# Optimization experiments

Hardware: AMD Instinct MI355X
Metric: run time of the kernel (lower is better)

## Reference

```python
import jax, jax.numpy as jnp
import numpy as np

D_MODEL = 1024
NUM_HEADS = 16
HEAD_DIM = D_MODEL // NUM_HEADS


def setup_inputs() -> dict:
    key = jax.random.key(0)
    k0, k1, k2, k3, k4 = jax.random.split(key, 5)
    B, S, D = 4, 2048, D_MODEL
    std = np.sqrt(2.0 / (D + D)).astype(np.float32)
    return {
        "in_features": jax.random.normal(k0, (B, S, D), dtype=jnp.float32),
        "Wq": jax.random.normal(k1, (D, D), dtype=jnp.float32) * std,
        "Wk": jax.random.normal(k2, (D, D), dtype=jnp.float32) * std,
        "Wv": jax.random.normal(k3, (D, D), dtype=jnp.float32) * std,
        "Wo": jax.random.normal(k4, (D, D), dtype=jnp.float32) * std,
    }


def reference(in_features, Wq, Wk, Wv, Wo):
    B, S, D = in_features.shape
    H, Hd = NUM_HEADS, HEAD_DIM

    def split_heads(x):  # (B,S,D) -> (B,H,S,Hd)
        return x.reshape(B, S, H, Hd).transpose(0, 2, 1, 3)

    q = split_heads(in_features @ Wq.T)
    k = split_heads(in_features @ Wk.T)
    v = split_heads(in_features @ Wv.T)

    scale = 1.0 / jnp.sqrt(jnp.asarray(Hd, dtype=q.dtype))
    scores = jnp.einsum("bhsd,bhtd->bhst", q, k) * scale  # (B,H,S,S)
    causal = jnp.tril(jnp.ones((S, S), dtype=bool))  # (S,S)
    scores = jnp.where(causal[None, None], scores, -jnp.inf)
    attn = jax.nn.softmax(scores, axis=-1)
    out = jnp.einsum("bhst,bhtd->bhsd", attn, v)  # (B,H,S,Hd)
    out = out.transpose(0, 2, 1, 3).reshape(B, S, D)
    return out @ Wo.T
```

## Files before the change

kernel.cpp:

```cpp
#include <hip/hip_runtime.h>


typedef float f32x4 __attribute__((ext_vector_type(4)));
typedef short s16x8 __attribute__((ext_vector_type(8)));

#if __has_builtin(__builtin_amdgcn_exp2f)
#define EXP2(x) __builtin_amdgcn_exp2f(x)
#else
#define EXP2(x) exp2f(x)
#endif

__device__ __forceinline__ unsigned short f2bf(float f) {
  unsigned int u = __float_as_uint(f);
  u += 0x7fffu + ((u >> 16) & 1u);
  return (unsigned short)(u >> 16);
}

__device__ __forceinline__ unsigned int pk2bf(float f0, float f1) {
  return __builtin_amdgcn_perm(__float_as_uint(f1) + 0x8000u,
                               __float_as_uint(f0) + 0x8000u, 0x07060302u);
}

__device__ __forceinline__ void gl_lds16(const short* g, short* lds) {
  __builtin_amdgcn_global_load_lds(
      (const __attribute__((address_space(1))) unsigned int*)g,
      (__attribute__((address_space(3))) unsigned int*)lds, 16, 0, 0);
}

__global__ __launch_bounds__(256) void cvt_kernel(const float4* __restrict__ s,
                                                  ushort4* __restrict__ d, int n4) {
  int i = blockIdx.x * blockDim.x + threadIdx.x;
  int stride = gridDim.x * blockDim.x;
  for (int idx = i; idx < n4; idx += stride) {
    float4 f = s[idx];
    ushort4 r;
    r.x = f2bf(f.x); r.y = f2bf(f.y); r.z = f2bf(f.z); r.w = f2bf(f.w);
    d[idx] = r;
  }
}

__global__ __launch_bounds__(256) void cvtw_kernel(const float4* __restrict__ w0,
                                                   const float4* __restrict__ w1,
                                                   const float4* __restrict__ w2,
                                                   const float4* __restrict__ w3,
                                                   ushort4* __restrict__ d0,
                                                   ushort4* __restrict__ d1,
                                                   ushort4* __restrict__ d2,
                                                   ushort4* __restrict__ d3) {
  const int n4 = 1024 * 1024 / 4;
  const float4* s;
  ushort4* d;
  switch (blockIdx.y) {
    case 0: s = w0; d = d0; break;
    case 1: s = w1; d = d1; break;
    case 2: s = w2; d = d2; break;
    default: s = w3; d = d3; break;
  }
  int i = blockIdx.x * blockDim.x + threadIdx.x;
  int stride = gridDim.x * blockDim.x;
  for (int idx = i; idx < n4; idx += stride) {
    float4 f = s[idx];
    ushort4 r;
    r.x = f2bf(f.x); r.y = f2bf(f.y); r.z = f2bf(f.z); r.w = f2bf(f.w);
    d[idx] = r;
  }
}

template <int MODE>
__global__ __launch_bounds__(256) void gemm_bt(const short* __restrict__ A,
                                               const short* __restrict__ B,
                                               float* __restrict__ Cf,
                                               short* __restrict__ q_o,
                                               short* __restrict__ k_o,
                                               short* __restrict__ vT_o,
                                               int M, int N, int K) {
  const int tid = threadIdx.x;
  const int wave = tid >> 6, lane = tid & 63;
  const int quad = lane >> 4, l15 = lane & 15;
  const int m0 = blockIdx.x * 128, n0 = blockIdx.y * 128;
  const int wm = (wave >> 1) * 64, wn = (wave & 1) * 64;

  __shared__ __align__(16) short As[128 * 64];
  __shared__ __align__(16) short Bs[128 * 64];

  const f32x4 z4 = {0.f, 0.f, 0.f, 0.f};
  f32x4 acc[4][4];
  for (int i = 0; i < 4; ++i)
    for (int j = 0; j < 4; ++j) acc[i][j] = z4;

  for (int k0 = 0; k0 < K; k0 += 64) {
    __syncthreads();
    for (int i = 0; i < 4; ++i) {
      int c = wave * 4 + i;
      int r = c * 8 + (lane >> 3);
      int c8 = (lane & 7) ^ (r & 7);
      gl_lds16(A + (size_t)(m0 + r) * K + k0 + c8 * 8, As + c * 512 + lane * 8);
      gl_lds16(B + (size_t)(n0 + r) * K + k0 + c8 * 8, Bs + c * 512 + lane * 8);
    }
    __syncthreads();
    for (int kk = 0; kk < 64; kk += 32) {
      int c8b = (kk >> 3) + quad;
      s16x8 af[4], bfr[4];
      for (int mt = 0; mt < 4; ++mt) {
        int row = wm + mt * 16 + l15;
        af[mt] = *(const s16x8*)(As + row * 64 + ((c8b ^ (row & 7)) << 3));
      }
      for (int nt = 0; nt < 4; ++nt) {
        int row = wn + nt * 16 + l15;
        bfr[nt] = *(const s16x8*)(Bs + row * 64 + ((c8b ^ (row & 7)) << 3));
      }
      for (int mt = 0; mt < 4; ++mt)
        for (int nt = 0; nt < 4; ++nt)
          acc[mt][nt] = __builtin_amdgcn_mfma_f32_16x16x32_bf16(af[mt], bfr[nt],
                                                                acc[mt][nt], 0, 0, 0);
    }
  }

  if (MODE == 0) {
    for (int mt = 0; mt < 4; ++mt)
      for (int nt = 0; nt < 4; ++nt) {
        int col = n0 + wn + nt * 16 + l15;
        for (int r = 0; r < 4; ++r) {
          int row = m0 + wm + mt * 16 + quad * 4 + r;
          Cf[(size_t)row * N + col] = acc[mt][nt][r];
        }
      }
  } else {
    if (n0 < 1024) {
      const float scale = 0.18033688011112042f;
      for (int mt = 0; mt < 4; ++mt)
        for (int nt = 0; nt < 4; ++nt) {
          int col = n0 + wn + nt * 16 + l15;
          for (int r = 0; r < 4; ++r) {
            int row = m0 + wm + mt * 16 + quad * 4 + r;
            ((unsigned short*)q_o)[(size_t)row * 1024 + col] = f2bf(acc[mt][nt][r] * scale);
          }
        }
    } else if (n0 < 2048) {
      for (int mt = 0; mt < 4; ++mt)
        for (int nt = 0; nt < 4; ++nt) {
          int col = n0 - 1024 + wn + nt * 16 + l15;
          for (int r = 0; r < 4; ++r) {
            int row = m0 + wm + mt * 16 + quad * 4 + r;
            ((unsigned short*)k_o)[(size_t)row * 1024 + col] = f2bf(acc[mt][nt][r]);
          }
        }
    } else {
      for (int mt = 0; mt < 4; ++mt)
        for (int nt = 0; nt < 4; ++nt) {
          int col = n0 - 2048 + wn + nt * 16 + l15;
          int h = col >> 6, d = col & 63;
          int row0 = m0 + wm + mt * 16 + quad * 4;
          int b = row0 >> 11, s = row0 & 2047;
          uint2 pk;
          pk.x = pk2bf(acc[mt][nt][0], acc[mt][nt][1]);
          pk.y = pk2bf(acc[mt][nt][2], acc[mt][nt][3]);
          *(uint2*)((unsigned short*)vT_o + (((size_t)b * 16 + h) * 64 + d) * 2048 + s) = pk;
        }
    }
  }
}

__global__ __launch_bounds__(256) void attn_kernel(const short* __restrict__ qb,
                                                   const short* __restrict__ kb,
                                                   const short* __restrict__ vT,
                                                   short* __restrict__ ob) {
  const int p = blockIdx.x;
  const int bh = blockIdx.y;
  const int tid = threadIdx.x;
  const int wave = tid >> 6, lane = tid & 63;
  const int quad = lane >> 4, l15 = lane & 15;
  const size_t rowbase = (size_t)(bh >> 4) * 2048;
  const int hoff = (bh & 15) * 64;

  __shared__ __align__(16) short Ks[8192];
  __shared__ __align__(16) short VTs[8192];
  __shared__ __align__(16) short Ps[10240];
  short* Pw = Ps + wave * 2560;

  const f32x4 z4 = {0.f, 0.f, 0.f, 0.f};

  for (int pass = 0; pass < 2; ++pass) {
    const int qt = pass ? p : 15 - p;
    const int q0 = qt * 128;

    s16x8 qf[2][2];
#pragma unroll
    for (int n = 0; n < 2; ++n) {
      const short* qrow = qb + (rowbase + q0 + wave * 32 + n * 16 + l15) * 1024 + hoff;
#pragma unroll
      for (int k2 = 0; k2 < 2; ++k2)
        qf[n][k2] = *(const s16x8*)(qrow + k2 * 32 + quad * 8);
    }

    f32x4 oacc[2][4];
#pragma unroll
    for (int n = 0; n < 2; ++n)
#pragma unroll
      for (int dt = 0; dt < 4; ++dt) oacc[n][dt] = z4;
    float lacc[2] = {0.f, 0.f};

    for (int t = 0; t <= qt; ++t) {
      __syncthreads();
#pragma unroll
      for (int i = 0; i < 4; ++i) {
        int c = wave * 4 + i;
        int r = c * 8 + (lane >> 3);
        int c8 = (lane & 7) ^ (r & 7);
        gl_lds16(kb + (rowbase + t * 128 + r) * 1024 + hoff + c8 * 8, Ks + c * 512 + lane * 8);
      }
#pragma unroll
      for (int i = 0; i < 4; ++i) {
        int c = wave * 4 + i;
        int d = c * 4 + (lane >> 4);
        int c8 = (lane & 15) ^ (d & 7);
        gl_lds16(vT + ((size_t)bh * 64 + d) * 2048 + t * 128 + c8 * 8, VTs + c * 512 + lane * 8);
      }
      __syncthreads();

      f32x4 sacc[2][8];
#pragma unroll
      for (int n = 0; n < 2; ++n)
#pragma unroll
        for (int m = 0; m < 8; ++m) sacc[n][m] = z4;
#pragma unroll
      for (int k2 = 0; k2 < 2; ++k2) {
#pragma unroll
        for (int m = 0; m < 8; ++m) {
          int row = m * 16 + l15;
          s16x8 kf = *(const s16x8*)(Ks + row * 64 + ((((k2 << 2) + quad) ^ (row & 7)) << 3));
          sacc[0][m] = __builtin_amdgcn_mfma_f32_16x16x32_bf16(kf, qf[0][k2], sacc[0][m], 0, 0, 0);
          sacc[1][m] = __builtin_amdgcn_mfma_f32_16x16x32_bf16(kf, qf[1][k2], sacc[1][m], 0, 0, 0);
        }
      }

      if (t == qt) {
#pragma unroll
        for (int n = 0; n < 2; ++n) {
          int qg = wave * 32 + n * 16 + l15;
#pragma unroll
          for (int m = 0; m < 8; ++m) {
            int kvb = m * 16 + quad * 4;
#pragma unroll
            for (int r = 0; r < 4; ++r)
              if (kvb + r > qg) sacc[n][m][r] = -1e30f;
          }
        }
      }

      uint2 pp[2][8];
#pragma unroll
      for (int n = 0; n < 2; ++n) {
        float sum = 0.f;
#pragma unroll
        for (int m = 0; m < 8; ++m) {
          float p0 = EXP2(sacc[n][m][0]);
          float p1 = EXP2(sacc[n][m][1]);
          float p2 = EXP2(sacc[n][m][2]);
          float p3 = EXP2(sacc[n][m][3]);
          sum += (p0 + p1) + (p2 + p3);
          pp[n][m].x = pk2bf(p0, p1);
          pp[n][m].y = pk2bf(p2, p3);
        }
        lacc[n] += sum;
      }

#pragma unroll
      for (int kk = 0; kk < 4; ++kk) {
        short* Pb = Pw + (kk & 1) * 1280;
#pragma unroll
        for (int n = 0; n < 2; ++n)
#pragma unroll
          for (int mm = 0; mm < 2; ++mm)
            *(uint2*)(Pb + (n * 16 + l15) * 40 + mm * 16 + quad * 4) = pp[n][2 * kk + mm];
        s16x8 pf0 = *(const s16x8*)(Pb + l15 * 40 + quad * 8);
        s16x8 pf1 = *(const s16x8*)(Pb + (16 + l15) * 40 + quad * 8);
#pragma unroll
        for (int dt = 0; dt < 4; ++dt) {
          int d = dt * 16 + l15;
          s16x8 vf = *(const s16x8*)(VTs + d * 128 + ((((kk << 2) + quad) ^ (d & 7)) << 3));
          oacc[0][dt] = __builtin_amdgcn_mfma_f32_16x16x32_bf16(vf, pf0, oacc[0][dt], 0, 0, 0);
          oacc[1][dt] = __builtin_amdgcn_mfma_f32_16x16x32_bf16(vf, pf1, oacc[1][dt], 0, 0, 0);
        }
      }
    }

#pragma unroll
    for (int n = 0; n < 2; ++n) {
      float l = lacc[n];
      l += __shfl_xor(l, 16);
      l += __shfl_xor(l, 32);
      float inv = 1.0f / l;
      size_t row = rowbase + q0 + wave * 32 + n * 16 + l15;
      unsigned short* orow = (unsigned short*)ob + row * 1024 + hoff;
#pragma unroll
      for (int dt = 0; dt < 4; ++dt) {
        f32x4 v = oacc[n][dt];
        uint2 pk;
        pk.x = pk2bf(v[0] * inv, v[1] * inv);
        pk.y = pk2bf(v[2] * inv, v[3] * inv);
        *(uint2*)(orow + dt * 16 + quad * 4) = pk;
      }
    }
  }
}

extern "C" void kernel_launch(void* const* d_in, const int* in_sizes, int n_in,
                              void* d_out, int out_size, void* d_ws, size_t ws_size,
                              hipStream_t stream) {
  const float* X  = (const float*)d_in[0];
  const float* Wq = (const float*)d_in[1];
  const float* Wk = (const float*)d_in[2];
  const float* Wv = (const float*)d_in[3];
  const float* Wo = (const float*)d_in[4];

  short* xb   = (short*)d_ws;
  short* wqkv = xb + (size_t)8192 * 1024;
  short* wob  = wqkv + (size_t)3072 * 1024;
  short* qb   = wob + (size_t)1024 * 1024;
  short* kb   = qb + (size_t)8192 * 1024;
  short* vT   = kb + (size_t)8192 * 1024;
  short* ob   = xb;

  const int MB = 8192;

  cvt_kernel<<<2048, 256, 0, stream>>>((const float4*)X, (ushort4*)xb, MB * 1024 / 4);
  cvtw_kernel<<<dim3(128, 4), 256, 0, stream>>>(
      (const float4*)Wq, (const float4*)Wk, (const float4*)Wv, (const float4*)Wo,
      (ushort4*)wqkv, (ushort4*)(wqkv + 1024 * 1024), (ushort4*)(wqkv + 2 * 1024 * 1024),
      (ushort4*)wob);

  gemm_bt<1><<<dim3(64, 24), 256, 0, stream>>>(xb, wqkv, nullptr, qb, kb, vT, MB, 3072, 1024);

  attn_kernel<<<dim3(8, 64), 256, 0, stream>>>(qb, kb, vT, ob);

  gemm_bt<0><<<dim3(64, 8), 256, 0, stream>>>(ob, wob, (float*)d_out, nullptr, nullptr,
                                              nullptr, MB, 1024, 1024);
}
```

Measured before the change: 277.0 us.

## Load K/V fragments directly from global memory, one q-tile per block

```diff
diff --git a/kernel.cpp b/kernel.cpp
--- a/kernel.cpp
+++ b/kernel.cpp
@@ -161,146 +161,126 @@
   }
 }
 
-__global__ __launch_bounds__(256) void attn_kernel(const short* __restrict__ qb,
-                                                   const short* __restrict__ kb,
-                                                   const short* __restrict__ vT,
-                                                   short* __restrict__ ob) {
-  const int p = blockIdx.x;
-  const int bh = blockIdx.y;
+__global__ __launch_bounds__(256, 3) void attn_kernel(const short* __restrict__ qb,
+                                                      const short* __restrict__ kb,
+                                                      const short* __restrict__ vT,
+                                                      short* __restrict__ ob) {
+  const int bh = blockIdx.x;
+  const int qt = 15 - (int)blockIdx.y;
   const int tid = threadIdx.x;
   const int wave = tid >> 6, lane = tid & 63;
   const int quad = lane >> 4, l15 = lane & 15;
+  const int q0 = qt * 128;
   const size_t rowbase = (size_t)(bh >> 4) * 2048;
   const int hoff = (bh & 15) * 64;
 
-  __shared__ __align__(16) short Ks[8192];
-  __shared__ __align__(16) short VTs[8192];
   __shared__ __align__(16) short Ps[10240];
   short* Pw = Ps + wave * 2560;
 
+  const short* kp = kb + (rowbase + l15) * 1024 + hoff + quad * 8;
+  const short* vp = vT + ((size_t)bh * 64 + l15) * 2048 + quad * 8;
+
+  s16x8 qf[2][2];
+#pragma unroll
+  for (int n = 0; n < 2; ++n) {
+    const short* qrow = qb + (rowbase + q0 + wave * 32 + n * 16 + l15) * 1024 + hoff;
+#pragma unroll
+    for (int k2 = 0; k2 < 2; ++k2)
+      qf[n][k2] = *(const s16x8*)(qrow + k2 * 32 + quad * 8);
+  }
+
   const f32x4 z4 = {0.f, 0.f, 0.f, 0.f};
-
-  for (int pass = 0; pass < 2; ++pass) {
-    const int qt = pass ? p : 15 - p;
-    const int q0 = qt * 128;
-
-    s16x8 qf[2][2];
+  f32x4 oacc[2][4];
+#pragma unroll
+  for (int n = 0; n < 2; ++n)
+#pragma unroll
+    for (int dt = 0; dt < 4; ++dt) oacc[n][dt] = z4;
+  float lacc[2] = {0.f, 0.f};
+
+  for (int t = 0; t <= qt; ++t) {
+    const short* kt = kp + (size_t)t * 128 * 1024;
+    const short* vt = vp + t * 128;
+
+    f32x4 sacc[2][8];
+#pragma unroll
+    for (int n = 0; n < 2; ++n)
+#pragma unroll
+      for (int m = 0; m < 8; ++m) sacc[n][m] = z4;
+#pragma unroll
+    for (int k2 = 0; k2 < 2; ++k2) {
+#pragma unroll
+      for (int m = 0; m < 8; ++m) {
+        s16x8 kf = *(const s16x8*)(kt + m * 16 * 1024 + k2 * 32);
+        sacc[0][m] = __builtin_amdgcn_mfma_f32_16x16x32_bf16(kf, qf[0][k2], sacc[0][m], 0, 0, 0);
+        sacc[1][m] = __builtin_amdgcn_mfma_f32_16x16x32_bf16(kf, qf[1][k2], sacc[1][m], 0, 0, 0);
+      }
+    }
+
+    if (t == qt) {
+#pragma unroll
+      for (int n = 0; n < 2; ++n) {
+        int qg = wave * 32 + n * 16 + l15;
+#pragma unroll
+        for (int m = 0; m < 8; ++m) {
+          int kvb = m * 16 + quad * 4;
+#pragma unroll
+          for (int r = 0; r < 4; ++r)
+            if (kvb + r > qg) sacc[n][m][r] = -1e30f;
+        }
+      }
+    }
+
+    uint2 pp[2][8];
 #pragma unroll
     for (int n = 0; n < 2; ++n) {
-      const short* qrow = qb + (rowbase + q0 + wave * 32 + n * 16 + l15) * 1024 + hoff;
-#pragma unroll
-      for (int k2 = 0; k2 < 2; ++k2)
-        qf[n][k2] = *(const s16x8*)(qrow + k2 * 32 + quad * 8);
-    }
-
-    f32x4 oacc[2][4];
-#pragma unroll
-    for (int n = 0; n < 2; ++n)
-#pragma unroll
-      for (int dt = 0; dt < 4; ++dt) oacc[n][dt] = z4;
-    float lacc[2] = {0.f, 0.f};
-
-    for (int t = 0; t <= qt; ++t) {
-      __syncthreads();
-#pragma unroll
-      for (int i = 0; i < 4; ++i) {
-        int c = wave * 4 + i;
-        int r = c * 8 + (lane >> 3);
-        int c8 = (lane & 7) ^ (r & 7);
-        gl_lds16(kb + (rowbase + t * 128 + r) * 1024 + hoff + c8 * 8, Ks + c * 512 + lane * 8);
-      }
-#pragma unroll
-      for (int i = 0; i < 4; ++i) {
-        int c = wave * 4 + i;
-        int d = c * 4 + (lane >> 4);
-        int c8 = (lane & 15) ^ (d & 7);
-        gl_lds16(vT + ((size_t)bh * 64 + d) * 2048 + t * 128 + c8 * 8, VTs + c * 512 + lane * 8);
-      }
-      __syncthreads();
-
-      f32x4 sacc[2][8];
+      float sum = 0.f;
+#pragma unroll
+      for (int m = 0; m < 8; ++m) {
+        float p0 = EXP2(sacc[n][m][0]);
+        float p1 = EXP2(sacc[n][m][1]);
+        float p2 = EXP2(sacc[n][m][2]);
+        float p3 = EXP2(sacc[n][m][3]);
+        sum += (p0 + p1) + (p2 + p3);
+        pp[n][m].x = pk2bf(p0, p1);
+        pp[n][m].y = pk2bf(p2, p3);
+      }
+      lacc[n] += sum;
+    }
+
+#pragma unroll
+    for (int kk = 0; kk < 4; ++kk) {
+      short* Pb = Pw + (kk & 1) * 1280;
 #pragma unroll
       for (int n = 0; n < 2; ++n)
 #pragma unroll
-        for (int m = 0; m < 8; ++m) sacc[n][m] = z4;
-#pragma unroll
-      for (int k2 = 0; k2 < 2; ++k2) {
-#pragma unroll
-        for (int m = 0; m < 8; ++m) {
-          int row = m * 16 + l15;
-          s16x8 kf = *(const s16x8*)(Ks + row * 64 + ((((k2 << 2) + quad) ^ (row & 7)) << 3));
-          sacc[0][m] = __builtin_amdgcn_mfma_f32_16x16x32_bf16(kf, qf[0][k2], sacc[0][m], 0, 0, 0);
-          sacc[1][m] = __builtin_amdgcn_mfma_f32_16x16x32_bf16(kf, qf[1][k2], sacc[1][m], 0, 0, 0);
-        }
-      }
-
-      if (t == qt) {
-#pragma unroll
-        for (int n = 0; n < 2; ++n) {
-          int qg = wave * 32 + n * 16 + l15;
-#pragma unroll
-          for (int m = 0; m < 8; ++m) {
-            int kvb = m * 16 + quad * 4;
-#pragma unroll
-            for (int r = 0; r < 4; ++r)
-              if (kvb + r > qg) sacc[n][m][r] = -1e30f;
-          }
-        }
-      }
-
-      uint2 pp[2][8];
-#pragma unroll
-      for (int n = 0; n < 2; ++n) {
-        float sum = 0.f;
-#pragma unroll
-        for (int m = 0; m < 8; ++m) {
-          float p0 = EXP2(sacc[n][m][0]);
-          float p1 = EXP2(sacc[n][m][1]);
-          float p2 = EXP2(sacc[n][m][2]);
-          float p3 = EXP2(sacc[n][m][3]);
-          sum += (p0 + p1) + (p2 + p3);
-          pp[n][m].x = pk2bf(p0, p1);
-          pp[n][m].y = pk2bf(p2, p3);
-        }
-        lacc[n] += sum;
-      }
-
-#pragma unroll
-      for (int kk = 0; kk < 4; ++kk) {
-        short* Pb = Pw + (kk & 1) * 1280;
-#pragma unroll
-        for (int n = 0; n < 2; ++n)
-#pragma unroll
-          for (int mm = 0; mm < 2; ++mm)
-            *(uint2*)(Pb + (n * 16 + l15) * 40 + mm * 16 + quad * 4) = pp[n][2 * kk + mm];
-        s16x8 pf0 = *(const s16x8*)(Pb + l15 * 40 + quad * 8);
-        s16x8 pf1 = *(const s16x8*)(Pb + (16 + l15) * 40 + quad * 8);
-#pragma unroll
-        for (int dt = 0; dt < 4; ++dt) {
-          int d = dt * 16 + l15;
-          s16x8 vf = *(const s16x8*)(VTs + d * 128 + ((((kk << 2) + quad) ^ (d & 7)) << 3));
-          oacc[0][dt] = __builtin_amdgcn_mfma_f32_16x16x32_bf16(vf, pf0, oacc[0][dt], 0, 0, 0);
-          oacc[1][dt] = __builtin_amdgcn_mfma_f32_16x16x32_bf16(vf, pf1, oacc[1][dt], 0, 0, 0);
-        }
-      }
-    }
-
-#pragma unroll
-    for (int n = 0; n < 2; ++n) {
-      float l = lacc[n];
-      l += __shfl_xor(l, 16);
-      l += __shfl_xor(l, 32);
-      float inv = 1.0f / l;
-      size_t row = rowbase + q0 + wave * 32 + n * 16 + l15;
-      unsigned short* orow = (unsigned short*)ob + row * 1024 + hoff;
+        for (int mm = 0; mm < 2; ++mm)
+          *(uint2*)(Pb + (n * 16 + l15) * 40 + mm * 16 + quad * 4) = pp[n][2 * kk + mm];
+      s16x8 pf0 = *(const s16x8*)(Pb + l15 * 40 + quad * 8);
+      s16x8 pf1 = *(const s16x8*)(Pb + (16 + l15) * 40 + quad * 8);
 #pragma unroll
       for (int dt = 0; dt < 4; ++dt) {
-        f32x4 v = oacc[n][dt];
-        uint2 pk;
-        pk.x = pk2bf(v[0] * inv, v[1] * inv);
-        pk.y = pk2bf(v[2] * inv, v[3] * inv);
-        *(uint2*)(orow + dt * 16 + quad * 4) = pk;
-      }
+        s16x8 vf = *(const s16x8*)(vt + dt * 16 * 2048 + kk * 32);
+        oacc[0][dt] = __builtin_amdgcn_mfma_f32_16x16x32_bf16(vf, pf0, oacc[0][dt], 0, 0, 0);
+        oacc[1][dt] = __builtin_amdgcn_mfma_f32_16x16x32_bf16(vf, pf1, oacc[1][dt], 0, 0, 0);
+      }
+    }
+  }
+
+#pragma unroll
+  for (int n = 0; n < 2; ++n) {
+    float l = lacc[n];
+    l += __shfl_xor(l, 16);
+    l += __shfl_xor(l, 32);
+    float inv = 1.0f / l;
+    size_t row = rowbase + q0 + wave * 32 + n * 16 + l15;
+    unsigned short* orow = (unsigned short*)ob + row * 1024 + hoff;
+#pragma unroll
+    for (int dt = 0; dt < 4; ++dt) {
+      f32x4 v = oacc[n][dt];
+      uint2 pk;
+      pk.x = pk2bf(v[0] * inv, v[1] * inv);
+      pk.y = pk2bf(v[2] * inv, v[3] * inv);
+      *(uint2*)(orow + dt * 16 + quad * 4) = pk;
     }
   }
 }
@@ -332,7 +312,7 @@
 
   gemm_bt<1><<<dim3(64, 24), 256, 0, stream>>>(xb, wqkv, nullptr, qb, kb, vT, MB, 3072, 1024);
 
-  attn_kernel<<<dim3(8, 64), 256, 0, stream>>>(qb, kb, vT, ob);
+  attn_kernel<<<dim3(64, 16), 256, 0, stream>>>(qb, kb, vT, ob);
 
   gemm_bt<0><<<dim3(64, 8), 256, 0, stream>>>(ob, wob, (float*)d_out, nullptr, nullptr,
                                               nullptr, MB, 1024, 1024);
```

New measurement: 322.6 us. +16.5%, slower.
